# Kernel tuning notes

Measured on AMD Instinct MI355X. Metric: run time of the kernel, lower is better.

The kernel has to match this reference:

```python
import jax, jax.numpy as jnp
import numpy as np

# pywt 'db4' decomposition low-pass filter (orthogonal Daubechies-4, 8 taps)
_DB4_DEC_LO = np.array([
    -0.010597401784997278, 0.032883011666982945,
     0.030841381835986965, -0.18703481171888114,
    -0.02798376941698385,  0.6308807679295904,
     0.7148465705525415,   0.23037781330885523], dtype=np.float32)
_REC_LO = _DB4_DEC_LO[::-1].copy()                                   # reconstruction low-pass
_REC_HI = (_DB4_DEC_LO * ((-1.0) ** np.arange(8))).astype(np.float32)  # reconstruction high-pass
LEVEL = 3


def _iswt_level(lo, hi, w, dilation):
    """One inverse-SWT level: periodic a-trous synthesis, halved tight-frame dual.
    lo, hi: (BN, T); w: (1, 2, Lf) correlation kernel (rec filters pre-flipped)."""
    Lf = w.shape[-1]
    padl, padr = dilation * (Lf // 2), dilation * (Lf // 2 - 1)
    x = jnp.stack([lo, hi], axis=1)  # (BN, 2, T)
    x = jnp.pad(x, ((0, 0), (0, 0), (padl, padr)), mode="wrap")  # periodic boundary
    y = jax.lax.conv_general_dilated(
        x, w, window_strides=(1,), padding="VALID",
        rhs_dilation=(dilation,),
        dimension_numbers=("NCH", "OIH", "NCH"))  # (BN, 1, T)
    return 0.5 * y[:, 0, :]


def _iswt(coeffs):
    """coeffs: (B, N, T, level+1) with last dim ordered [cA_n, cD_n, ..., cD_1].
    Faithfully mirrors the torch module: it builds the list [cD_1,...,cD_n,cA_n]
    and hands it to ptwt.iswt, which treats element 0 as the running approximation
    and iterates the remaining bands with dilation 2**(n_details - pos - 1)."""
    B, N, T, nb = coeffs.shape
    c = coeffs.reshape(B * N, T, nb)
    w = jnp.stack([jnp.asarray(_REC_LO)[::-1],
                   jnp.asarray(_REC_HI)[::-1]])[None].astype(coeffs.dtype)  # (1,2,Lf)
    order = list(range(nb - 1, 0, -1)) + [0]  # [cD_1, ..., cD_n, cA_n]
    res_lo = c[:, :, order[0]]
    details = order[1:]
    for pos, idx in enumerate(details):
        dilation = 2 ** (len(details) - pos - 1)
        res_lo = _iswt_level(res_lo, c[:, :, idx], w, dilation)
    return res_lo.reshape(B, N, T)


def setup_inputs() -> dict:
    key = jax.random.key(0)
    coeffs = jax.random.normal(key, (32, 128, 4096, LEVEL + 1), dtype=jnp.float32)
    return {"coeffs": coeffs}


def reference(coeffs):
    return _iswt(coeffs)
```

## Files before the change

kernel.cpp:

```cpp
#include <hip/hip_runtime.h>

static constexpr float H0 = -0.010597401784997278f;
static constexpr float H1 =  0.032883011666982945f;
static constexpr float H2 =  0.030841381835986965f;
static constexpr float H3 = -0.18703481171888114f;
static constexpr float H4 = -0.02798376941698385f;
static constexpr float H5 =  0.6308807679295904f;
static constexpr float H6 =  0.7148465705525415f;
static constexpr float H7 =  0.23037781330885523f;

static constexpr float W0[8] = { 0.5f*H0,  0.5f*H1,  0.5f*H2,  0.5f*H3,
                                 0.5f*H4,  0.5f*H5,  0.5f*H6,  0.5f*H7 };
static constexpr float W1[8] = {-0.5f*H7,  0.5f*H6, -0.5f*H5,  0.5f*H4,
                                -0.5f*H3,  0.5f*H2, -0.5f*H1,  0.5f*H0 };

constexpr int T      = 4096;
constexpr int GMASK  = 1023;
constexpr int BANDF  = 5120;

static __device__ __forceinline__ int gaddr(int g) { return (g << 2) + ((g >> 2) << 2); }

template <int D, int NG>
static __device__ __forceinline__ void level(const float* __restrict__ lo_buf,
                                             const float* __restrict__ hi_buf,
                                             int g0, float res[16])
{
    float wl[NG * 4], wh[NG * 4];
#pragma unroll
    for (int j = 0; j < NG; ++j) {
        const int g = (g0 - D + j) & GMASK;
        const int a = gaddr(g);
        const float4 vl = *(const float4*)(lo_buf + a);
        const float4 vh = *(const float4*)(hi_buf + a);
        wl[4 * j + 0] = vl.x; wl[4 * j + 1] = vl.y; wl[4 * j + 2] = vl.z; wl[4 * j + 3] = vl.w;
        wh[4 * j + 0] = vh.x; wh[4 * j + 1] = vh.y; wh[4 * j + 2] = vh.z; wh[4 * j + 3] = vh.w;
    }
#pragma unroll
    for (int i = 0; i < 16; ++i) {
        float acc = 0.0f;
#pragma unroll
        for (int k = 0; k < 8; ++k) {
            acc = fmaf(W0[k], wl[i + D * k], acc);
            acc = fmaf(W1[k], wh[i + D * k], acc);
        }
        res[i] = acc;
    }
}

static __device__ __forceinline__ void writeback(float* __restrict__ dst, int g0,
                                                 const float res[16])
{
#pragma unroll
    for (int j = 0; j < 4; ++j) {
        const int a = gaddr(g0 + j);
        *(float4*)(dst + a) = make_float4(res[4 * j + 0], res[4 * j + 1],
                                          res[4 * j + 2], res[4 * j + 3]);
    }
}

__global__ __launch_bounds__(256, 2)
void iswt_kernel(const float* __restrict__ in, float* __restrict__ out)
{
    __shared__ float lds[4][BANDF];

    const int row = blockIdx.x;
    const int tid = threadIdx.x;

    const float4* __restrict__ src = (const float4*)(in + (size_t)row * (T * 4));
#pragma unroll
    for (int j = 0; j < 16; ++j) {
        const int p = tid + 256 * j;
        const float4 v = src[p];
        const int a = p + ((p >> 4) << 2);
        lds[0][a] = v.x;
        lds[1][a] = v.y;
        lds[2][a] = v.z;
        lds[3][a] = v.w;
    }
    __syncthreads();

    const int g0 = tid << 2;
    float res[16];

    level<4, 11>(&lds[3][0], &lds[2][0], g0, res);
    __syncthreads();
    writeback(&lds[3][0], g0, res);
    __syncthreads();

    level<2, 8>(&lds[3][0], &lds[1][0], g0, res);
    __syncthreads();
    writeback(&lds[1][0], g0, res);
    __syncthreads();

    level<1, 6>(&lds[1][0], &lds[0][0], g0, res);

    float* __restrict__ o = out + (size_t)row * T + (tid << 4);
#pragma unroll
    for (int j = 0; j < 4; ++j)
        *(float4*)(o + 4 * j) = make_float4(res[4 * j + 0], res[4 * j + 1],
                                            res[4 * j + 2], res[4 * j + 3]);
}

extern "C" void kernel_launch(void* const* d_in, const int* in_sizes, int n_in,
                              void* d_out, int out_size, void* d_ws, size_t ws_size,
                              hipStream_t stream)
{
    const float* coeffs = (const float*)d_in[0];
    float* out = (float*)d_out;
    const int nrows = in_sizes[0] / (T * 4);
    iswt_kernel<<<nrows, 256, 0, stream>>>(coeffs, out);
}
```

Baseline: 66.55 us.

## Process several rows per block with register-staged prefetch of next row

Each block now handles 8 rows in a loop instead of one. The next row's global loads go into registers while the current row's three synthesis levels run out of LDS. This is meant to hide global memory latency and cut block launch overhead. It costs 64 extra VGPRs per thread under launch_bounds(256,2), which may cause register pressure or spills, and the grid shrinks to nrows/8 blocks (512), which may leave many CUs underoccupied.

```diff
diff --git a/kernel.cpp b/kernel.cpp
--- a/kernel.cpp
+++ b/kernel.cpp
@@ -14,9 +14,10 @@
 static constexpr float W1[8] = {-0.5f*H7,  0.5f*H6, -0.5f*H5,  0.5f*H4,
                                 -0.5f*H3,  0.5f*H2, -0.5f*H1,  0.5f*H0 };
 
-constexpr int T      = 4096;
-constexpr int GMASK  = 1023;
-constexpr int BANDF  = 5120;
+constexpr int T     = 4096;
+constexpr int GMASK = 1023;
+constexpr int BANDF = 5120;
+constexpr int RPB   = 8;
 
 static __device__ __forceinline__ int gaddr(int g) { return (g << 2) + ((g >> 2) << 2); }
 
@@ -63,42 +64,58 @@
 {
     __shared__ float lds[4][BANDF];
 
-    const int row = blockIdx.x;
-    const int tid = threadIdx.x;
+    const int tid  = threadIdx.x;
+    const int row0 = blockIdx.x * RPB;
 
-    const float4* __restrict__ src = (const float4*)(in + (size_t)row * (T * 4));
+    float4 stage[16];
+    {
+        const float4* __restrict__ src = (const float4*)(in + (size_t)row0 * (T * 4));
 #pragma unroll
-    for (int j = 0; j < 16; ++j) {
-        const int p = tid + 256 * j;
-        const float4 v = src[p];
-        const int a = p + ((p >> 4) << 2);
-        lds[0][a] = v.x;
-        lds[1][a] = v.y;
-        lds[2][a] = v.z;
-        lds[3][a] = v.w;
+        for (int j = 0; j < 16; ++j) stage[j] = src[tid + 256 * j];
     }
-    __syncthreads();
 
-    const int g0 = tid << 2;
-    float res[16];
+    for (int i = 0; i < RPB; ++i) {
+        const int row = row0 + i;
 
-    level<4, 11>(&lds[3][0], &lds[2][0], g0, res);
-    __syncthreads();
-    writeback(&lds[3][0], g0, res);
-    __syncthreads();
+#pragma unroll
+        for (int j = 0; j < 16; ++j) {
+            const int p = tid + 256 * j;
+            const int a = p + ((p >> 4) << 2);
+            lds[0][a] = stage[j].x;
+            lds[1][a] = stage[j].y;
+            lds[2][a] = stage[j].z;
+            lds[3][a] = stage[j].w;
+        }
+        __syncthreads();
 
-    level<2, 8>(&lds[3][0], &lds[1][0], g0, res);
-    __syncthreads();
-    writeback(&lds[1][0], g0, res);
-    __syncthreads();
+        if (i + 1 < RPB) {
+            const float4* __restrict__ src = (const float4*)(in + (size_t)(row + 1) * (T * 4));
+#pragma unroll
+            for (int j = 0; j < 16; ++j) stage[j] = src[tid + 256 * j];
+        }
 
-    level<1, 6>(&lds[1][0], &lds[0][0], g0, res);
+        const int g0 = tid << 2;
+        float res[16];
 
-    float* __restrict__ o = out + (size_t)row * T + (tid << 4);
+        level<4, 11>(&lds[3][0], &lds[2][0], g0, res);
+        __syncthreads();
+        writeback(&lds[3][0], g0, res);
+        __syncthreads();
+
+        level<2, 8>(&lds[3][0], &lds[1][0], g0, res);
+        __syncthreads();
+        writeback(&lds[1][0], g0, res);
+        __syncthreads();
+
+        level<1, 6>(&lds[1][0], &lds[0][0], g0, res);
+
+        float* __restrict__ o = out + (size_t)row * T + (tid << 4);
 #pragma unroll
-    for (int j = 0; j < 4; ++j)
-        *(float4*)(o + 4 * j) = make_float4(res[4 * j + 0], res[4 * j + 1],
-                                            res[4 * j + 2], res[4 * j + 3]);
+        for (int j = 0; j < 4; ++j)
+            *(float4*)(o + 4 * j) = make_float4(res[4 * j + 0], res[4 * j + 1],
+                                                res[4 * j + 2], res[4 * j + 3]);
+        __syncthreads();
+    }
 }
 
 extern "C" void kernel_launch(void* const* d_in, const int* in_sizes, int n_in,
@@ -108,5 +125,5 @@
     const float* coeffs = (const float*)d_in[0];
     float* out = (float*)d_out;
     const int nrows = in_sizes[0] / (T * 4);
-    iswt_kernel<<<nrows, 256, 0, stream>>>(coeffs, out);
+    iswt_kernel<<<nrows / RPB, 256, 0, stream>>>(coeffs, out);
 }
```

After: 72.01 us. 1.08x slower.

## Split each row into four 1024-sample tiles with halo recomputation

Applied to the files above, without the earlier changes.

Each row is now processed by four blocks, each owning a 1024-sample output tile. A block loads a halo of surrounding coefficients and recomputes the overlap between levels so that no cross-block communication is needed. LDS use per block drops from 80KB to about 21KB, and launch bounds rise to 5 blocks per CU, which raises occupancy and grid size to hide memory latency. In exchange, about 6% of input is loaded twice and some halo work is computed redundantly.

```diff
diff --git a/kernel.cpp b/kernel.cpp
--- a/kernel.cpp
+++ b/kernel.cpp
@@ -14,29 +14,29 @@
 static constexpr float W1[8] = {-0.5f*H7,  0.5f*H6, -0.5f*H5,  0.5f*H4,
                                 -0.5f*H3,  0.5f*H2, -0.5f*H1,  0.5f*H0 };
 
-constexpr int T      = 4096;
-constexpr int GMASK  = 1023;
-constexpr int BANDF  = 5120;
+constexpr int T     = 4096;
+constexpr int TILE  = 1024;
+constexpr int SG    = 272;
+constexpr int BANDF = 1360;
 
-static __device__ __forceinline__ int gaddr(int g) { return (g << 2) + ((g >> 2) << 2); }
+static __device__ __forceinline__ int paddr(int g) { return (g << 2) + ((g >> 2) << 2); }
 
 template <int D, int NG>
-static __device__ __forceinline__ void level(const float* __restrict__ lo_buf,
-                                             const float* __restrict__ hi_buf,
-                                             int g0, float res[16])
+static __device__ __forceinline__ void level1g(const float* __restrict__ lo,
+                                               const float* __restrict__ hi,
+                                               int lg, float res[4])
 {
     float wl[NG * 4], wh[NG * 4];
 #pragma unroll
     for (int j = 0; j < NG; ++j) {
-        const int g = (g0 - D + j) & GMASK;
-        const int a = gaddr(g);
-        const float4 vl = *(const float4*)(lo_buf + a);
-        const float4 vh = *(const float4*)(hi_buf + a);
+        const int a = paddr(lg - D + j);
+        const float4 vl = *(const float4*)(lo + a);
+        const float4 vh = *(const float4*)(hi + a);
         wl[4 * j + 0] = vl.x; wl[4 * j + 1] = vl.y; wl[4 * j + 2] = vl.z; wl[4 * j + 3] = vl.w;
         wh[4 * j + 0] = vh.x; wh[4 * j + 1] = vh.y; wh[4 * j + 2] = vh.z; wh[4 * j + 3] = vh.w;
     }
 #pragma unroll
-    for (int i = 0; i < 16; ++i) {
+    for (int i = 0; i < 4; ++i) {
         float acc = 0.0f;
 #pragma unroll
         for (int k = 0; k < 8; ++k) {
@@ -47,58 +47,58 @@
     }
 }
 
-static __device__ __forceinline__ void writeback(float* __restrict__ dst, int g0,
-                                                 const float res[16])
+static __device__ __forceinline__ void wr4(float* __restrict__ dst, int lg, const float r[4])
 {
-#pragma unroll
-    for (int j = 0; j < 4; ++j) {
-        const int a = gaddr(g0 + j);
-        *(float4*)(dst + a) = make_float4(res[4 * j + 0], res[4 * j + 1],
-                                          res[4 * j + 2], res[4 * j + 3]);
-    }
+    *(float4*)(dst + paddr(lg)) = make_float4(r[0], r[1], r[2], r[3]);
 }
 
-__global__ __launch_bounds__(256, 2)
+__global__ __launch_bounds__(256, 5)
 void iswt_kernel(const float* __restrict__ in, float* __restrict__ out)
 {
     __shared__ float lds[4][BANDF];
 
-    const int row = blockIdx.x;
-    const int tid = threadIdx.x;
+    const int tid  = threadIdx.x;
+    const int bid  = blockIdx.x;
+    const int row  = bid >> 2;
+    const int t0   = (bid & 3) << 10;
 
     const float4* __restrict__ src = (const float4*)(in + (size_t)row * (T * 4));
 #pragma unroll
-    for (int j = 0; j < 16; ++j) {
-        const int p = tid + 256 * j;
-        const float4 v = src[p];
-        const int a = p + ((p >> 4) << 2);
-        lds[0][a] = v.x;
-        lds[1][a] = v.y;
-        lds[2][a] = v.z;
-        lds[3][a] = v.w;
+    for (int j = 0; j < 4; ++j) {
+        const int fp = tid + (j << 8);
+        const int P  = (t0 - 32 + fp) & (T - 1);
+        const float4 v = src[P];
+        const int a  = fp + ((fp >> 4) << 2);
+        lds[0][a] = v.x; lds[1][a] = v.y; lds[2][a] = v.z; lds[3][a] = v.w;
+    }
+    if (tid < 64) {
+        const int fp = 1024 + tid;
+        const int P  = (t0 - 32 + fp) & (T - 1);
+        const float4 v = src[P];
+        const int a  = fp + ((fp >> 4) << 2);
+        lds[0][a] = v.x; lds[1][a] = v.y; lds[2][a] = v.z; lds[3][a] = v.w;
     }
     __syncthreads();
 
-    const int g0 = tid << 2;
-    float res[16];
-
-    level<4, 11>(&lds[3][0], &lds[2][0], g0, res);
+    float ra[4], rb[4];
+    level1g<4, 8>(&lds[3][0], &lds[2][0], 4 + tid, ra);
+    if (tid < 8) level1g<4, 8>(&lds[3][0], &lds[2][0], 260 + tid, rb);
     __syncthreads();
-    writeback(&lds[3][0], g0, res);
+    wr4(&lds[3][0], 4 + tid, ra);
+    if (tid < 8) wr4(&lds[3][0], 260 + tid, rb);
     __syncthreads();
 
-    level<2, 8>(&lds[3][0], &lds[1][0], g0, res);
+    level1g<2, 5>(&lds[3][0], &lds[1][0], 6 + tid, ra);
+    if (tid < 4) level1g<2, 5>(&lds[3][0], &lds[1][0], 262 + tid, rb);
     __syncthreads();
-    writeback(&lds[1][0], g0, res);
+    wr4(&lds[1][0], 6 + tid, ra);
+    if (tid < 4) wr4(&lds[1][0], 262 + tid, rb);
     __syncthreads();
 
-    level<1, 6>(&lds[1][0], &lds[0][0], g0, res);
-
-    float* __restrict__ o = out + (size_t)row * T + (tid << 4);
-#pragma unroll
-    for (int j = 0; j < 4; ++j)
-        *(float4*)(o + 4 * j) = make_float4(res[4 * j + 0], res[4 * j + 1],
-                                            res[4 * j + 2], res[4 * j + 3]);
+    float r3[4];
+    level1g<1, 3>(&lds[1][0], &lds[0][0], 8 + tid, r3);
+    *(float4*)(out + (size_t)row * T + t0 + (tid << 2)) =
+        make_float4(r3[0], r3[1], r3[2], r3[3]);
 }
 
 extern "C" void kernel_launch(void* const* d_in, const int* in_sizes, int n_in,
@@ -108,5 +108,5 @@
     const float* coeffs = (const float*)d_in[0];
     float* out = (float*)d_out;
     const int nrows = in_sizes[0] / (T * 4);
-    iswt_kernel<<<nrows, 256, 0, stream>>>(coeffs, out);
+    iswt_kernel<<<nrows * 4, 256, 0, stream>>>(coeffs, out);
 }
```

After: 86.40 us. 29.8% more time.

## Split rows into halo tiles and double-buffer global-to-LDS loads across tiles

Applied to the files above, without the earlier changes.

Each row is split into two 2048-sample tiles with halos. Each block handles four tiles and uses direct global_load_lds with double buffering, so the next tile's load overlaps the current tile's three synthesis levels. The transposed float4 register loads are replaced by per-band scalar DMA loads, and a separate scratch buffer holds the intermediate level. This adds halo recomputation and manual vmcnt/lgkmcnt waits, and it cuts the grid size by a factor of two.

```diff
diff --git a/kernel.cpp b/kernel.cpp
--- a/kernel.cpp
+++ b/kernel.cpp
@@ -14,91 +14,104 @@
 static constexpr float W1[8] = {-0.5f*H7,  0.5f*H6, -0.5f*H5,  0.5f*H4,
                                 -0.5f*H3,  0.5f*H2, -0.5f*H1,  0.5f*H0 };
 
-constexpr int T      = 4096;
-constexpr int GMASK  = 1023;
-constexpr int BANDF  = 5120;
-
-static __device__ __forceinline__ int gaddr(int g) { return (g << 2) + ((g >> 2) << 2); }
+constexpr int T  = 4096;
+constexpr int BD = 2112;
+constexpr int NT = 4;
 
 template <int D, int NG>
-static __device__ __forceinline__ void level(const float* __restrict__ lo_buf,
-                                             const float* __restrict__ hi_buf,
-                                             int g0, float res[16])
+static __device__ __forceinline__ void lvl(const float* __restrict__ lo,
+                                           const float* __restrict__ hi,
+                                           int lg, float r[4])
 {
     float wl[NG * 4], wh[NG * 4];
 #pragma unroll
     for (int j = 0; j < NG; ++j) {
-        const int g = (g0 - D + j) & GMASK;
-        const int a = gaddr(g);
-        const float4 vl = *(const float4*)(lo_buf + a);
-        const float4 vh = *(const float4*)(hi_buf + a);
-        wl[4 * j + 0] = vl.x; wl[4 * j + 1] = vl.y; wl[4 * j + 2] = vl.z; wl[4 * j + 3] = vl.w;
-        wh[4 * j + 0] = vh.x; wh[4 * j + 1] = vh.y; wh[4 * j + 2] = vh.z; wh[4 * j + 3] = vh.w;
+        const float4 vl = *(const float4*)(lo + 4 * (lg - D + j));
+        const float4 vh = *(const float4*)(hi + 4 * (lg - D + j));
+        wl[4*j+0] = vl.x; wl[4*j+1] = vl.y; wl[4*j+2] = vl.z; wl[4*j+3] = vl.w;
+        wh[4*j+0] = vh.x; wh[4*j+1] = vh.y; wh[4*j+2] = vh.z; wh[4*j+3] = vh.w;
     }
 #pragma unroll
-    for (int i = 0; i < 16; ++i) {
-        float acc = 0.0f;
+    for (int jp = 0; jp < 4; ++jp) {
+        float a = 0.0f;
 #pragma unroll
         for (int k = 0; k < 8; ++k) {
-            acc = fmaf(W0[k], wl[i + D * k], acc);
-            acc = fmaf(W1[k], wh[i + D * k], acc);
+            a = fmaf(W0[k], wl[jp + D * k], a);
+            a = fmaf(W1[k], wh[jp + D * k], a);
         }
-        res[i] = acc;
+        r[jp] = a;
     }
 }
 
-static __device__ __forceinline__ void writeback(float* __restrict__ dst, int g0,
-                                                 const float res[16])
-{
-#pragma unroll
-    for (int j = 0; j < 4; ++j) {
-        const int a = gaddr(g0 + j);
-        *(float4*)(dst + a) = make_float4(res[4 * j + 0], res[4 * j + 1],
-                                          res[4 * j + 2], res[4 * j + 3]);
-    }
-}
+static __device__ __forceinline__ void st4(float* __restrict__ p, const float r[4])
+{ *(float4*)p = make_float4(r[0], r[1], r[2], r[3]); }
 
 __global__ __launch_bounds__(256, 2)
 void iswt_kernel(const float* __restrict__ in, float* __restrict__ out)
 {
-    __shared__ float lds[4][BANDF];
+    __shared__ __align__(16) float bands[2][4][BD];
+    __shared__ __align__(16) float S[BD];
 
-    const int row = blockIdx.x;
-    const int tid = threadIdx.x;
+    const int t    = threadIdx.x;
+    const int wv   = t >> 6;
+    const int lane = t & 63;
+    const int tile0 = blockIdx.x * NT;
 
-    const float4* __restrict__ src = (const float4*)(in + (size_t)row * (T * 4));
-#pragma unroll
-    for (int j = 0; j < 16; ++j) {
-        const int p = tid + 256 * j;
-        const float4 v = src[p];
-        const int a = p + ((p >> 4) << 2);
-        lds[0][a] = v.x;
-        lds[1][a] = v.y;
-        lds[2][a] = v.z;
-        lds[3][a] = v.w;
+    auto issue = [&](int set, int tile) {
+        const int row = tile >> 1;
+        const int t0  = (tile & 1) << 11;
+        const float* rb = in + (size_t)row * (T * 4);
+        for (int c = 0; c < 33; ++c) {
+            const int p = (t0 - 28 + (c << 6) + lane) & (T - 1);
+            __builtin_amdgcn_global_load_lds(
+                (const __attribute__((address_space(1))) void*)(rb + 4 * p + wv),
+                (__attribute__((address_space(3))) void*)(&bands[set][wv][c << 6]),
+                4, 0, 0);
+        }
+    };
+
+    issue(0, tile0);
+    int cur = 0;
+
+    for (int i = 0; i < NT; ++i) {
+        const int tile = tile0 + i;
+        const int row  = tile >> 1;
+        const int t0   = (tile & 1) << 11;
+
+        if (i + 1 < NT) {
+            issue(cur ^ 1, tile + 1);
+            asm volatile("s_waitcnt vmcnt(33)" ::: "memory");
+        } else {
+            asm volatile("s_waitcnt vmcnt(0)" ::: "memory");
+        }
+        __builtin_amdgcn_s_barrier();
+
+        const float* cA  = bands[cur][0];
+        const float* cD3 = bands[cur][1];
+        const float* cD2 = bands[cur][2];
+        float*       cD1 = bands[cur][3];
+        float r[4];
+
+        lvl<4, 8>(cD1, cD2, 4 + t, r);    st4(S + 4 * (4 + t), r);
+        lvl<4, 8>(cD1, cD2, 260 + t, r);  st4(S + 4 * (260 + t), r);
+        if (t < 6) { lvl<4, 8>(cD1, cD2, 516 + t, r); st4(S + 4 * (516 + t), r); }
+        asm volatile("s_waitcnt lgkmcnt(0)" ::: "memory");
+        __builtin_amdgcn_s_barrier();
+
+        lvl<2, 5>(S, cD3, 6 + t, r);      st4(cD1 + 4 * (6 + t), r);
+        lvl<2, 5>(S, cD3, 262 + t, r);    st4(cD1 + 4 * (262 + t), r);
+        if (t < 2) { lvl<2, 5>(S, cD3, 518 + t, r); st4(cD1 + 4 * (518 + t), r); }
+        asm volatile("s_waitcnt lgkmcnt(0)" ::: "memory");
+        __builtin_amdgcn_s_barrier();
+
+        float* orow = out + (size_t)row * T + t0;
+        lvl<1, 3>(cD1, cA, 7 + t, r);     st4(orow + 4 * t, r);
+        lvl<1, 3>(cD1, cA, 263 + t, r);   st4(orow + 1024 + 4 * t, r);
+        asm volatile("s_waitcnt lgkmcnt(0)" ::: "memory");
+        __builtin_amdgcn_s_barrier();
+
+        cur ^= 1;
     }
-    __syncthreads();
-
-    const int g0 = tid << 2;
-    float res[16];
-
-    level<4, 11>(&lds[3][0], &lds[2][0], g0, res);
-    __syncthreads();
-    writeback(&lds[3][0], g0, res);
-    __syncthreads();
-
-    level<2, 8>(&lds[3][0], &lds[1][0], g0, res);
-    __syncthreads();
-    writeback(&lds[1][0], g0, res);
-    __syncthreads();
-
-    level<1, 6>(&lds[1][0], &lds[0][0], g0, res);
-
-    float* __restrict__ o = out + (size_t)row * T + (tid << 4);
-#pragma unroll
-    for (int j = 0; j < 4; ++j)
-        *(float4*)(o + 4 * j) = make_float4(res[4 * j + 0], res[4 * j + 1],
-                                            res[4 * j + 2], res[4 * j + 3]);
 }
 
 extern "C" void kernel_launch(void* const* d_in, const int* in_sizes, int n_in,
@@ -107,6 +120,7 @@
 {
     const float* coeffs = (const float*)d_in[0];
     float* out = (float*)d_out;
-    const int nrows = in_sizes[0] / (T * 4);
-    iswt_kernel<<<nrows, 256, 0, stream>>>(coeffs, out);
+    const int nrows  = in_sizes[0] / (T * 4);
+    const int blocks = nrows * 2 / NT;
+    iswt_kernel<<<blocks, 256, 0, stream>>>(coeffs, out);
 }
```

New measurement: 103.7 us. 1.56x slower.
